# Performance work log

Hardware: AMD Instinct MI355X
Metric: run time of the kernel (lower is better)

Reference implementation:

```python
import jax, jax.numpy as jnp
import numpy as np

NT = 50000  # target nodes
ND = 50000  # drug nodes
E = 800000  # edges per relation
F = 128     # raw feature dim
C = 64      # hidden channels
NEG_SLOPE = 0.2


def _gat(x_src, x_dst, ei, W_src, W_dst, a_src, a_dst, b, n_dst):
    """PyG GATConv (heads=1, add_self_loops=False) forward."""
    hs = x_src @ W_src                      # [Ns, C]
    hd = x_dst @ W_dst                      # [Nd, C]
    alpha_s = hs @ a_src                    # [Ns]
    alpha_d = hd @ a_dst                    # [Nd]
    src, dst = ei[0], ei[1]
    logits = jax.nn.leaky_relu(alpha_s[src] + alpha_d[dst], NEG_SLOPE)  # [E]
    # segment softmax over incoming edges of each dst node
    m = jax.ops.segment_max(logits, dst, num_segments=n_dst)
    ex = jnp.exp(logits - m[dst])
    den = jax.ops.segment_sum(ex, dst, num_segments=n_dst)
    w = ex / (den[dst] + 1e-16)
    out = jax.ops.segment_sum(w[:, None] * hs[src], dst, num_segments=n_dst)
    return out + b


def setup_inputs() -> dict:
    key = jax.random.key(0)
    ks = jax.random.split(key, 32)
    d = {
        "x_target": jax.random.normal(ks[0], (NT, F), jnp.float32),
        "x_drug": jax.random.normal(ks[1], (ND, F), jnp.float32),
        "ei_tt": jax.random.randint(ks[2], (2, E), 0, NT),
        "ei_dt": jnp.stack([jax.random.randint(ks[3], (E,), 0, ND),
                            jax.random.randint(ks[4], (E,), 0, NT)]),
        "ei_dd": jax.random.randint(ks[5], (2, E), 0, ND),
        "ei_td": jnp.stack([jax.random.randint(ks[6], (E,), 0, NT),
                            jax.random.randint(ks[7], (E,), 0, ND)]),
        "W_tt": jax.random.normal(ks[8], (F, C), jnp.float32) * 0.1,
        "att_tt_src": jax.random.normal(ks[9], (C,), jnp.float32) * 0.1,
        "att_tt_dst": jax.random.normal(ks[10], (C,), jnp.float32) * 0.1,
        "b_tt": jnp.zeros((C,), jnp.float32),
        "W_dt_src": jax.random.normal(ks[11], (F, C), jnp.float32) * 0.1,
        "W_dt_dst": jax.random.normal(ks[12], (F, C), jnp.float32) * 0.1,
        "att_dt_src": jax.random.normal(ks[13], (C,), jnp.float32) * 0.1,
        "att_dt_dst": jax.random.normal(ks[14], (C,), jnp.float32) * 0.1,
        "b_dt": jnp.zeros((C,), jnp.float32),
        "W_dd": jax.random.normal(ks[15], (F, C), jnp.float32) * 0.1,
        "att_dd_src": jax.random.normal(ks[16], (C,), jnp.float32) * 0.1,
        "att_dd_dst": jax.random.normal(ks[17], (C,), jnp.float32) * 0.1,
        "b_dd": jnp.zeros((C,), jnp.float32),
        "W_td_src": jax.random.normal(ks[18], (C, C), jnp.float32) * 0.1,
        "W_td_dst": jax.random.normal(ks[19], (F, C), jnp.float32) * 0.1,
        "att_td_src": jax.random.normal(ks[20], (C,), jnp.float32) * 0.1,
        "att_td_dst": jax.random.normal(ks[21], (C,), jnp.float32) * 0.1,
        "b_td": jnp.zeros((C,), jnp.float32),
    }
    return d


def reference(x_target, x_drug, ei_tt, ei_dt, ei_dd, ei_td,
              W_tt, att_tt_src, att_tt_dst, b_tt,
              W_dt_src, W_dt_dst, att_dt_src, att_dt_dst, b_dt,
              W_dd, att_dd_src, att_dd_dst, b_dd,
              W_td_src, W_td_dst, att_td_src, att_td_dst, b_td):
    x_tt = _gat(x_target, x_target, ei_tt, W_tt, W_tt, att_tt_src, att_tt_dst, b_tt, NT)
    x_dt = _gat(x_drug, x_target, ei_dt, W_dt_src, W_dt_dst, att_dt_src, att_dt_dst, b_dt, NT)
    x_target_new = (x_tt + x_dt) * 0.5
    x_dd = _gat(x_drug, x_drug, ei_dd, W_dd, W_dd, att_dd_src, att_dd_dst, b_dd, ND)
    x_td = _gat(x_target_new, x_drug, ei_td, W_td_src, W_td_dst, att_td_src, att_td_dst, b_td, ND)
    x_drug_new = (x_dd + x_td) * 0.5
    return x_target_new, x_drug_new
```

## Files before the change

### kernel.cpp

```cpp
#include <hip/hip_runtime.h>
#include <hip/hip_bf16.h>

typedef __hip_bfloat16 bf16;

typedef __bf16 bf16v8 __attribute__((ext_vector_type(8)));
typedef short  s16v8  __attribute__((ext_vector_type(8)));
typedef float  f32v4  __attribute__((ext_vector_type(4)));

#define NBLK  256
#define NBLKL 8

__device__ __forceinline__ float bf2f(unsigned short u) {
    return __uint_as_float(((unsigned)u) << 16);
}
__device__ __forceinline__ float bflo(unsigned v) {
    return __uint_as_float(v << 16);
}
__device__ __forceinline__ float bfhi(unsigned v) {
    return __uint_as_float(v & 0xFFFF0000u);
}
__device__ __forceinline__ float ldx(const void* p, size_t i, bool f32) {
    return f32 ? ((const float*)p)[i] : bf2f(((const unsigned short*)p)[i]);
}
__device__ __forceinline__ unsigned short f2bfbits(float f) {
    union { bf16 h; unsigned short u; } cv;
    cv.h = __float2bfloat16(f);
    return cv.u;
}
__device__ __forceinline__ float wave_sum(float v) {
    #pragma unroll
    for (int o = 32; o > 0; o >>= 1) v += __shfl_xor(v, o);
    return v;
}
__device__ __forceinline__ int physidx(int l, int NBtot) {
    return (l & (NBLK - 1)) * NBtot + (l >> NBLKL);
}

__global__ void detect_kernel(const unsigned* __restrict__ x, int nwords,
                              int* __restrict__ flag)
{
    __shared__ int cnt;
    if (threadIdx.x == 0) cnt = 0;
    __syncthreads();
    int c = 0;
    for (int i = threadIdx.x; i < nwords; i += blockDim.x) {
        unsigned e = (x[i] >> 23) & 0xFFu;
        if (e >= 100u && e <= 150u) c++;
    }
    atomicAdd(&cnt, c);
    __syncthreads();
    if (threadIdx.x == 0) flag[0] = (2 * cnt > nwords) ? 1 : 0;
}

struct RelSet {
    const int *src0, *dst0, *src1, *dst1, *src2, *dst2, *src3, *dst3;
    int off1, off2, off3, off4;
    int nd0, nd1, nd2, nd3;
};

__device__ __forceinline__ void pick(const RelSet& rs, int e, int& r,
                                     const int*& s, const int*& d, int& le)
{
    if (e < rs.off1)      { r = 0; s = rs.src0; d = rs.dst0; le = e; }
    else if (e < rs.off2) { r = 1; s = rs.src1; d = rs.dst1; le = e - rs.off1; }
    else if (e < rs.off3) { r = 2; s = rs.src2; d = rs.dst2; le = e - rs.off2; }
    else                  { r = 3; s = rs.src3; d = rs.dst3; le = e - rs.off3; }
}
__device__ __forceinline__ int ndst_of(const RelSet& rs, int r)
{
    return r == 0 ? rs.nd0 : r == 1 ? rs.nd1 : r == 2 ? rs.nd2 : rs.nd3;
}

__global__ __launch_bounds__(1024) void pass1_kernel(
    RelSet rs, int* __restrict__ hist, int NBr)
{
    extern __shared__ int lh[];
    const int NBtot = 4 * NBr;
    for (int i = threadIdx.x; i < NBtot; i += 1024) lh[i] = 0;
    __syncthreads();
    for (int e = blockIdx.x * 1024 + threadIdx.x; e < rs.off4; e += NBLK * 1024) {
        int r, le; const int *s, *d;
        pick(rs, e, r, s, d, le);
        atomicAdd(&lh[r * NBr + (d[le] >> 7)], 1);
    }
    __syncthreads();
    for (int i = threadIdx.x; i < NBtot; i += 1024)
        hist[blockIdx.x * NBtot + i] = lh[i];
}

__global__ __launch_bounds__(1024) void gscan_a_kernel(
    int* __restrict__ buf, int n, int NBtot, int* __restrict__ partials)
{
    __shared__ int sh[1024];
    const int t = threadIdx.x;
    const int base = blockIdx.x * 4096 + t * 4;
    int p0 = 0, p1 = 0, p2 = 0, p3 = 0;
    int v0 = 0, v1 = 0, v2 = 0, v3 = 0;
    if (base < n)     { p0 = physidx(base,     NBtot); v0 = buf[p0]; }
    if (base + 1 < n) { p1 = physidx(base + 1, NBtot); v1 = buf[p1]; }
    if (base + 2 < n) { p2 = physidx(base + 2, NBtot); v2 = buf[p2]; }
    if (base + 3 < n) { p3 = physidx(base + 3, NBtot); v3 = buf[p3]; }
    const int tsum = v0 + v1 + v2 + v3;
    sh[t] = tsum;
    __syncthreads();
    for (int o = 1; o < 1024; o <<= 1) {
        int u = (t >= o) ? sh[t - o] : 0;
        __syncthreads();
        sh[t] += u;
        __syncthreads();
    }
    const int texcl = sh[t] - tsum;
    if (base < n)     buf[p0] = texcl;
    if (base + 1 < n) buf[p1] = texcl + v0;
    if (base + 2 < n) buf[p2] = texcl + v0 + v1;
    if (base + 3 < n) buf[p3] = texcl + v0 + v1 + v2;
    if (t == 1023) partials[blockIdx.x] = sh[t];
}

__global__ __launch_bounds__(1024) void gscan_b_kernel(int* __restrict__ partials,
                                                       int nb)
{
    __shared__ int sh[1024];
    const int t = threadIdx.x;
    int v = (t < nb) ? partials[t] : 0;
    sh[t] = v;
    __syncthreads();
    for (int o = 1; o < 1024; o <<= 1) {
        int u = (t >= o) ? sh[t - o] : 0;
        __syncthreads();
        sh[t] += u;
        __syncthreads();
    }
    if (t < nb) partials[t] = sh[t] - v;
}

__global__ void gscan_c_kernel(int* __restrict__ buf,
                               const int* __restrict__ partials, int n, int NBtot)
{
    int l = blockIdx.x * blockDim.x + threadIdx.x;
    if (l < n) buf[physidx(l, NBtot)] += partials[l >> 12];
}

__global__ __launch_bounds__(1024) void scatter_kernel(
    RelSet rs, const int* __restrict__ O, unsigned* __restrict__ temp, int NBr)
{
    extern __shared__ int cur[];
    const int NBtot = 4 * NBr;
    for (int i = threadIdx.x; i < NBtot; i += 1024)
        cur[i] = O[blockIdx.x * NBtot + i];
    __syncthreads();
    for (int e = blockIdx.x * 1024 + threadIdx.x; e < rs.off4; e += NBLK * 1024) {
        int r, le; const int *s, *d;
        pick(rs, e, r, s, d, le);
        int dd = d[le];
        int b = r * NBr + (dd >> 7);
        int pos = atomicAdd(&cur[b], 1);
        temp[pos] = (unsigned)s[le] | ((unsigned)(dd & 127) << 16);
    }
}

__global__ __launch_bounds__(256) void fillb_kernel(
    RelSet rs, const int* __restrict__ O, const unsigned* __restrict__ temp,
    int* __restrict__ rowptr4, unsigned short* __restrict__ esrc4,
    int NBr, int NP, int EP, int TE)
{
    __shared__ int cnt[128];
    __shared__ int cur[128];
    const int b = blockIdx.x;
    const int NBtot = 4 * NBr;
    const int r = b / NBr;
    const int bloc = b - r * NBr;
    const int dbase = bloc << 7;
    const int nd = ndst_of(rs, r);
    const int bstart = O[b];
    const int bend   = (b + 1 < NBtot) ? O[b + 1] : TE;
    const int relstart = O[r * NBr];
    const int relend   = (r + 1 < 4) ? O[(r + 1) * NBr] : TE;
    const int t = threadIdx.x;

    if (t < 128) cnt[t] = 0;
    __syncthreads();
    for (int i = bstart + t; i < bend; i += 256)
        atomicAdd(&cnt[temp[i] >> 16], 1);
    __syncthreads();
    const int orig = (t < 128) ? cnt[t] : 0;
    for (int o = 1; o < 128; o <<= 1) {
        int add = 0;
        if (t < 128 && t >= o) add = cnt[t - o];
        __syncthreads();
        if (t < 128) cnt[t] += add;
        __syncthreads();
    }
    const int bucket_base = bstart - relstart;
    if (t < 128) {
        const int excl = cnt[t] - orig;
        cur[t] = bucket_base + excl;
        const int d = dbase + t;
        if (d < nd) rowptr4[r * (NP + 1) + d] = bucket_base + excl;
    }
    if (t == 0 && bloc == NBr - 1)
        rowptr4[r * (NP + 1) + nd] = relend - relstart;
    __syncthreads();
    unsigned short* es = esrc4 + (size_t)r * EP;
    for (int i = bstart + t; i < bend; i += 256) {
        unsigned u = temp[i];
        int pos = atomicAdd(&cur[u >> 16], 1);
        es[pos] = (unsigned short)(u & 0xFFFFu);
    }
}

__device__ __forceinline__ void pack_one(const void* W, unsigned short* Wp,
                                         int i, bool f32)
{
    int k = i >> 6, c = i & 63;
    int kt = k >> 5, q = (k >> 3) & 3, j = k & 7;
    int ct = c >> 4, n = c & 15;
    Wp[(((kt * 4 + ct) * 64) + q * 16 + n) * 8 + j] = f2bfbits(ldx(W, i, f32));
}

__global__ __launch_bounds__(256) void pack4_kernel(
    const void* __restrict__ W0, const void* __restrict__ W1,
    const void* __restrict__ W2, const void* __restrict__ W3,
    unsigned short* __restrict__ P0, unsigned short* __restrict__ P1,
    unsigned short* __restrict__ P2, unsigned short* __restrict__ P3,
    const int* __restrict__ flag)
{
    const bool f32 = (flag[0] != 0);
    int i = blockIdx.x * 256 + threadIdx.x;
    if (i < 8192)       pack_one(W0, P0, i, f32);
    else if (i < 16384) pack_one(W1, P1, i - 8192, f32);
    else if (i < 24576) pack_one(W2, P2, i - 16384, f32);
    else if (i < 28672) pack_one(W3, P3, i - 24576, f32);
}

__global__ void wvec2_kernel(const void* __restrict__ W1, const void* __restrict__ a1,
                             const void* __restrict__ W2, const void* __restrict__ a2,
                             float* __restrict__ wv1, float* __restrict__ wv2,
                             const int* __restrict__ flag)
{
    const bool f32 = (flag[0] != 0);
    const int t = threadIdx.x;
    const void* W = (t < 128) ? W1 : W2;
    const void* a = (t < 128) ? a1 : a2;
    const int k = t & 127;
    float s = 0.f;
    for (int c = 0; c < 64; ++c) s += ldx(W, (size_t)k * 64 + c, f32) * ldx(a, c, f32);
    ((t < 128) ? wv1 : wv2)[k] = s;
}

struct ProjArg {
    const void* X; const unsigned short* Wp; const void* a1; const void* a2;
    const float* wvx;
    bf16* H; float* al1; float* al2; float* alx;
    int N;
};

template <int K>
__device__ __forceinline__ void proj_body(const ProjArg& P, bool f32,
                                          int bid, int nblocks)
{
    constexpr int NKT = K / 32;
    const int tid = threadIdx.x;
    const int wave = tid >> 6, lane = tid & 63;
    const int quad = lane >> 4, n = lane & 15;

    s16v8 Bf[NKT][4];
    #pragma unroll
    for (int kt = 0; kt < NKT; ++kt)
        #pragma unroll
        for (int ct = 0; ct < 4; ++ct)
            Bf[kt][ct] = *(const s16v8*)&P.Wp[((kt * 4 + ct) * 64 + lane) * 8];

    float a1v[4], a2v[4];
    #pragma unroll
    for (int ct = 0; ct < 4; ++ct) {
        a1v[ct] = P.a1 ? ldx(P.a1, ct * 16 + n, f32) : 0.f;
        a2v[ct] = P.a2 ? ldx(P.a2, ct * 16 + n, f32) : 0.f;
    }
    float wv[NKT][8];
    if (P.wvx) {
        #pragma unroll
        for (int kt = 0; kt < NKT; ++kt)
            #pragma unroll
            for (int j = 0; j < 8; ++j)
                wv[kt][j] = P.wvx[kt * 32 + quad * 8 + j];
    }

    const int tiles = (P.N + 15) / 16;
    for (int tb = bid * 4 + wave; tb < tiles; tb += nblocks * 4) {
        const int r0 = tb * 16;
        const int arow = r0 + n;
        const int ars  = (arow < P.N) ? arow : 0;

        f32v4 acc[4];
        #pragma unroll
        for (int ct = 0; ct < 4; ++ct) acc[ct] = (f32v4){0.f, 0.f, 0.f, 0.f};
        float txd = 0.f;

        #pragma unroll
        for (int kt = 0; kt < NKT; ++kt) {
            s16v8 As;
            if (f32) {
                const float4* xp = (const float4*)P.X +
                    ((size_t)ars * K + kt * 32 + quad * 8) / 4;
                float4 x0 = xp[0], x1 = xp[1];
                As[0] = (short)f2bfbits(x0.x); As[1] = (short)f2bfbits(x0.y);
                As[2] = (short)f2bfbits(x0.z); As[3] = (short)f2bfbits(x0.w);
                As[4] = (short)f2bfbits(x1.x); As[5] = (short)f2bfbits(x1.y);
                As[6] = (short)f2bfbits(x1.z); As[7] = (short)f2bfbits(x1.w);
            } else {
                As = *(const s16v8*)((const unsigned short*)P.X +
                    (size_t)ars * K + kt * 32 + quad * 8);
            }
            if (P.wvx) {
                #pragma unroll
                for (int j = 0; j < 8; ++j)
                    txd = fmaf(bf2f((unsigned short)As[j]), wv[kt][j], txd);
            }
            bf16v8 Ab = __builtin_bit_cast(bf16v8, As);
            #pragma unroll
            for (int ct = 0; ct < 4; ++ct)
                acc[ct] = __builtin_amdgcn_mfma_f32_16x16x32_bf16(
                    Ab, __builtin_bit_cast(bf16v8, Bf[kt][ct]), acc[ct], 0, 0, 0);
        }

        if (P.alx) {
            txd += __shfl_xor(txd, 16);
            txd += __shfl_xor(txd, 32);
            if (lane < 16 && r0 + lane < P.N) P.alx[r0 + lane] = txd;
        }

        #pragma unroll
        for (int i = 0; i < 4; ++i) {
            const int r = r0 + quad * 4 + i;
            const bool rv = (r < P.N);
            if (rv && P.H) {
                #pragma unroll
                for (int ct = 0; ct < 4; ++ct)
                    P.H[(size_t)r * 64 + ct * 16 + n] = __float2bfloat16(acc[ct][i]);
            }
            if (P.al1) {
                float t = acc[0][i] * a1v[0] + acc[1][i] * a1v[1] +
                          acc[2][i] * a1v[2] + acc[3][i] * a1v[3];
                #pragma unroll
                for (int o = 1; o < 16; o <<= 1) t += __shfl_xor(t, o);
                if (rv && n == 0) P.al1[r] = t;
            }
            if (P.al2) {
                float t = acc[0][i] * a2v[0] + acc[1][i] * a2v[1] +
                          acc[2][i] * a2v[2] + acc[3][i] * a2v[3];
                #pragma unroll
                for (int o = 1; o < 16; o <<= 1) t += __shfl_xor(t, o);
                if (rv && n == 0) P.al2[r] = t;
            }
        }
    }
}

template <int KA, int KB, int KC>
__global__ __launch_bounds__(256) void proj3_kernel(ProjArg A, ProjArg B, ProjArg C,
                                                    int nA, int nB,
                                                    const int* __restrict__ flag)
{
    const bool f32 = (flag[0] != 0);
    const int bx = blockIdx.x;
    if (bx < nA)            proj_body<KA>(A, f32, bx, nA);
    else if (bx < nA + nB)  proj_body<KB>(B, f32, bx - nA, nB);
    else                    proj_body<KC>(C, f32, bx - nA - nB,
                                          gridDim.x - nA - nB);
}

template <int K>
__global__ __launch_bounds__(256) void proj1_kernel(ProjArg A,
                                                    const int* __restrict__ flag)
{
    proj_body<K>(A, flag[0] != 0, blockIdx.x, gridDim.x);
}

__global__ __launch_bounds__(256) void agg2_kernel(
    const int* __restrict__ rp1, const unsigned short* __restrict__ es1,
    const unsigned* __restrict__ HS1, const float* __restrict__ als1,
    const float* __restrict__ ald1,
    const int* __restrict__ rp2, const unsigned short* __restrict__ es2,
    const unsigned* __restrict__ HS2, const float* __restrict__ als2,
    const float* __restrict__ ald2,
    const void* __restrict__ b1, const void* __restrict__ b2,
    void* __restrict__ out, size_t out_off, int n, const int* __restrict__ flag)
{
    const int gw   = (blockIdx.x * blockDim.x + threadIdx.x) >> 6;
    const int lane = threadIdx.x & 63;
    if (gw >= n) return;
    const int half = lane >> 5;
    const int ch2  = lane & 31;

    int p1 = rp1[gw], e1 = rp1[gw + 1];
    int p2 = rp2[gw], e2 = rp2[gw + 1];
    const float ad1 = ald1[gw], ad2 = ald2[gw];

    float l1a = 0.f, h1a = 0.f, l1b = 0.f, h1b = 0.f, den1 = 0.f;
    float l2a = 0.f, h2a = 0.f, l2b = 0.f, h2b = 0.f, den2 = 0.f;

    while (p1 < e1 || p2 < e2) {
        int nn1 = e1 - p1; nn1 = nn1 < 0 ? 0 : (nn1 > 64 ? 64 : nn1);
        int nn2 = e2 - p2; nn2 = nn2 < 0 ? 0 : (nn2 > 64 ? 64 : nn2);
        int s1 = 0, s2 = 0; float w1 = 0.f, w2 = 0.f;
        if (lane < nn1) {
            s1 = es1[p1 + lane];
            float l = als1[s1] + ad1;
            l = (l > 0.f) ? l : 0.2f * l;
            w1 = __expf(l);
        }
        if (lane < nn2) {
            s2 = es2[p2 + lane];
            float l = als2[s2] + ad2;
            l = (l > 0.f) ? l : 0.2f * l;
            w2 = __expf(l);
        }
        den1 += w1; den2 += w2;

        const int jm = (nn1 > nn2) ? nn1 : nn2;
        for (int j = 0; j < jm; j += 8) {
            int   sA1 = __shfl(s1, j + half),     sB1 = __shfl(s1, j + 2 + half);
            int   sC1 = __shfl(s1, j + 4 + half), sD1 = __shfl(s1, j + 6 + half);
            float wA1 = __shfl(w1, j + half),     wB1 = __shfl(w1, j + 2 + half);
            float wC1 = __shfl(w1, j + 4 + half), wD1 = __shfl(w1, j + 6 + half);
            int   sA2 = __shfl(s2, j + half),     sB2 = __shfl(s2, j + 2 + half);
            int   sC2 = __shfl(s2, j + 4 + half), sD2 = __shfl(s2, j + 6 + half);
            float wA2 = __shfl(w2, j + half),     wB2 = __shfl(w2, j + 2 + half);
            float wC2 = __shfl(w2, j + 4 + half), wD2 = __shfl(w2, j + 6 + half);
            unsigned vA1 = HS1[(size_t)sA1 * 32 + ch2];
            unsigned vB1 = HS1[(size_t)sB1 * 32 + ch2];
            unsigned vC1 = HS1[(size_t)sC1 * 32 + ch2];
            unsigned vD1 = HS1[(size_t)sD1 * 32 + ch2];
            unsigned vA2 = HS2[(size_t)sA2 * 32 + ch2];
            unsigned vB2 = HS2[(size_t)sB2 * 32 + ch2];
            unsigned vC2 = HS2[(size_t)sC2 * 32 + ch2];
            unsigned vD2 = HS2[(size_t)sD2 * 32 + ch2];
            l1a = fmaf(wA1, bflo(vA1), l1a); h1a = fmaf(wA1, bfhi(vA1), h1a);
            l1b = fmaf(wB1, bflo(vB1), l1b); h1b = fmaf(wB1, bfhi(vB1), h1b);
            l1a = fmaf(wC1, bflo(vC1), l1a); h1a = fmaf(wC1, bfhi(vC1), h1a);
            l1b = fmaf(wD1, bflo(vD1), l1b); h1b = fmaf(wD1, bfhi(vD1), h1b);
            l2a = fmaf(wA2, bflo(vA2), l2a); h2a = fmaf(wA2, bfhi(vA2), h2a);
            l2b = fmaf(wB2, bflo(vB2), l2b); h2b = fmaf(wB2, bfhi(vB2), h2b);
            l2a = fmaf(wC2, bflo(vC2), l2a); h2a = fmaf(wC2, bfhi(vC2), h2a);
            l2b = fmaf(wD2, bflo(vD2), l2b); h2b = fmaf(wD2, bfhi(vD2), h2b);
        }
        p1 += nn1; p2 += nn2;
    }

    float lo1 = l1a + l1b, hi1 = h1a + h1b;
    float lo2 = l2a + l2b, hi2 = h2a + h2b;
    lo1 += __shfl_xor(lo1, 32); hi1 += __shfl_xor(hi1, 32);
    lo2 += __shfl_xor(lo2, 32); hi2 += __shfl_xor(hi2, 32);
    den1 = wave_sum(den1);
    den2 = wave_sum(den2);
    const float inv1 = 1.0f / (den1 + 1e-16f);
    const float inv2 = 1.0f / (den2 + 1e-16f);

    if (half == 0) {
        const bool f32 = (flag[0] != 0);
        const int c0 = 2 * ch2;
        float vlo = 0.5f * (lo1 * inv1 + lo2 * inv2 +
                            ldx(b1, c0, f32) + ldx(b2, c0, f32));
        float vhi = 0.5f * (hi1 * inv1 + hi2 * inv2 +
                            ldx(b1, c0 + 1, f32) + ldx(b2, c0 + 1, f32));
        const size_t pairidx = (out_off >> 1) + (size_t)gw * 32 + ch2;
        if (f32) ((float2*)out)[pairidx] = make_float2(vlo, vhi);
        else {
            ushort2 u2 = make_ushort2(f2bfbits(vlo), f2bfbits(vhi));
            ((ushort2*)out)[pairidx] = u2;
        }
    }
}

extern "C" void kernel_launch(void* const* d_in, const int* in_sizes, int n_in,
                              void* d_out, int out_size, void* d_ws, size_t ws_size,
                              hipStream_t stream)
{
    const void* x_t = d_in[0];
    const void* x_d = d_in[1];
    const int* ei_tt = (const int*)d_in[2];
    const int* ei_dt = (const int*)d_in[3];
    const int* ei_dd = (const int*)d_in[4];
    const int* ei_td = (const int*)d_in[5];
    const void* W_tt     = d_in[6];
    const void* att_tt_s = d_in[7];
    const void* att_tt_d = d_in[8];
    const void* b_tt     = d_in[9];
    const void* W_dt_src = d_in[10];
    const void* W_dt_dst = d_in[11];
    const void* att_dt_s = d_in[12];
    const void* att_dt_d = d_in[13];
    const void* b_dt     = d_in[14];
    const void* W_dd     = d_in[15];
    const void* att_dd_s = d_in[16];
    const void* att_dd_d = d_in[17];
    const void* b_dd     = d_in[18];
    const void* W_td_src = d_in[19];
    const void* W_td_dst = d_in[20];
    const void* att_td_s = d_in[21];
    const void* att_td_d = d_in[22];
    const void* b_td     = d_in[23];

    const int NT = in_sizes[0] / 128;
    const int ND = in_sizes[1] / 128;
    const int Ett = in_sizes[2] / 2, Edt = in_sizes[3] / 2,
              Edd = in_sizes[4] / 2, Etd = in_sizes[5] / 2;
    const int NMAX = (NT > ND) ? NT : ND;
    int EMAX = Ett;
    if (Edt > EMAX) EMAX = Edt;
    if (Edd > EMAX) EMAX = Edd;
    if (Etd > EMAX) EMAX = Etd;
    const int TE = Ett + Edt + Edd + Etd;

    const int NBr  = (NMAX + 127) >> 7;
    const int NBtot = 4 * NBr;
    const int HM = NBtot * NBLK;

    char* wptr = (char*)d_ws;
    auto alloc = [&](size_t bytes) -> void* {
        void* p = (void*)wptr;
        wptr += (bytes + 255) & ~(size_t)255;
        return p;
    };
    bf16*  h1      = (bf16*)alloc((size_t)NMAX * 64 * 2);
    bf16*  h2      = (bf16*)alloc((size_t)NMAX * 64 * 2);
    float* als[4]; float* ald[4];
    for (int r = 0; r < 4; ++r) {
        als[r] = (float*)alloc((size_t)NMAX * 4);
        ald[r] = (float*)alloc((size_t)NMAX * 4);
    }
    int*   hist    = (int*)alloc((size_t)HM * 4);
    int*   rowptr4 = (int*)alloc((size_t)4 * (NMAX + 1) * 4);
    unsigned short* esrc4 = (unsigned short*)alloc((size_t)4 * EMAX * 2);
    unsigned* temp = (unsigned*)alloc((size_t)TE * 4);
    int*   gpart   = (int*)alloc(1024 * 4);
    float* wvec_dt = (float*)alloc(128 * 4);
    float* wvec_td = (float*)alloc(128 * 4);
    unsigned short* wp_tt = (unsigned short*)alloc(8192 * 2);
    unsigned short* wp_dt = (unsigned short*)alloc(8192 * 2);
    unsigned short* wp_dd = (unsigned short*)alloc(8192 * 2);
    unsigned short* wp_td = (unsigned short*)alloc(4096 * 2);
    int*   flag    = (int*)alloc(256 * 4);
    bf16*  h3      = (bf16*)temp;

    RelSet rs;
    rs.src0 = ei_tt; rs.dst0 = ei_tt + Ett;
    rs.src1 = ei_dt; rs.dst1 = ei_dt + Edt;
    rs.src2 = ei_dd; rs.dst2 = ei_dd + Edd;
    rs.src3 = ei_td; rs.dst3 = ei_td + Etd;
    rs.off1 = Ett; rs.off2 = Ett + Edt; rs.off3 = Ett + Edt + Edd; rs.off4 = TE;
    rs.nd0 = NT; rs.nd1 = NT; rs.nd2 = ND; rs.nd3 = ND;

    detect_kernel<<<1, 256, 0, stream>>>((const unsigned*)x_t, 4096, flag);

    pack4_kernel<<<112, 256, 0, stream>>>(W_tt, W_dt_src, W_dd, W_td_src,
                                          wp_tt, wp_dt, wp_dd, wp_td, flag);
    wvec2_kernel<<<1, 256, 0, stream>>>(W_dt_dst, att_dt_d, W_td_dst, att_td_d,
                                        wvec_dt, wvec_td, flag);

    const size_t ldsB = (size_t)NBtot * 4;
    pass1_kernel<<<NBLK, 1024, ldsB, stream>>>(rs, hist, NBr);
    const int gnb = (HM + 4095) / 4096;
    gscan_a_kernel<<<gnb, 1024, 0, stream>>>(hist, HM, NBtot, gpart);
    gscan_b_kernel<<<1, 1024, 0, stream>>>(gpart, gnb);
    gscan_c_kernel<<<(HM + 255) / 256, 256, 0, stream>>>(hist, gpart, HM, NBtot);
    scatter_kernel<<<NBLK, 1024, ldsB, stream>>>(rs, hist, temp, NBr);
    fillb_kernel<<<NBtot, 256, 0, stream>>>(rs, hist, temp, rowptr4, esrc4,
                                            NBr, NMAX, EMAX, TE);

    ProjArg Ptt{ x_t, wp_tt, att_tt_s, att_tt_d, wvec_dt,
                 h1, als[0], ald[0], ald[1], NT };
    ProjArg Pdt{ x_d, wp_dt, att_dt_s, nullptr, wvec_td,
                 h2, als[1], nullptr, ald[3], ND };
    ProjArg Pdd{ x_d, wp_dd, att_dd_s, att_dd_d, nullptr,
                 h3, als[2], ald[2], nullptr, ND };
    proj3_kernel<128, 128, 128><<<2304, 256, 0, stream>>>(Ptt, Pdt, Pdd,
                                                          768, 768, flag);

    agg2_kernel<<<(NT + 3) / 4, 256, 0, stream>>>(
        rowptr4 + 0 * (NMAX + 1), esrc4 + (size_t)0 * EMAX,
        (const unsigned*)h1, als[0], ald[0],
        rowptr4 + 1 * (NMAX + 1), esrc4 + (size_t)1 * EMAX,
        (const unsigned*)h2, als[1], ald[1],
        b_tt, b_dt, d_out, 0, NT, flag);

    ProjArg Ptd{ d_out, wp_td, att_td_s, nullptr, nullptr,
                 h1, als[3], nullptr, nullptr, NT };
    proj1_kernel<64><<<1024, 256, 0, stream>>>(Ptd, flag);

    agg2_kernel<<<(ND + 3) / 4, 256, 0, stream>>>(
        rowptr4 + 2 * (NMAX + 1), esrc4 + (size_t)2 * EMAX,
        (const unsigned*)h3, als[2], ald[2],
        rowptr4 + 3 * (NMAX + 1), esrc4 + (size_t)3 * EMAX,
        (const unsigned*)h1, als[3], ald[3],
        b_dd, b_td, d_out, (size_t)NT * 64, ND, flag);
}
```

Baseline: 337.4 us.

## Replace two-level bucketed CSR build with global atomic counting sort

Result: slower. 625.2 us (+85.3%).

```diff
diff --git a/kernel.cpp b/kernel.cpp
--- a/kernel.cpp
+++ b/kernel.cpp
@@ -6,9 +6,6 @@
 typedef __bf16 bf16v8 __attribute__((ext_vector_type(8)));
 typedef short  s16v8  __attribute__((ext_vector_type(8)));
 typedef float  f32v4  __attribute__((ext_vector_type(4)));
-
-#define NBLK  256
-#define NBLKL 8
 
 __device__ __forceinline__ float bf2f(unsigned short u) {
     return __uint_as_float(((unsigned)u) << 16);
@@ -31,9 +28,6 @@
     #pragma unroll
     for (int o = 32; o > 0; o >>= 1) v += __shfl_xor(v, o);
     return v;
-}
-__device__ __forceinline__ int physidx(int l, int NBtot) {
-    return (l & (NBLK - 1)) * NBtot + (l >> NBLKL);
 }
 
 __global__ void detect_kernel(const unsigned* __restrict__ x, int nwords,
@@ -66,40 +60,34 @@
     else if (e < rs.off3) { r = 2; s = rs.src2; d = rs.dst2; le = e - rs.off2; }
     else                  { r = 3; s = rs.src3; d = rs.dst3; le = e - rs.off3; }
 }
-__device__ __forceinline__ int ndst_of(const RelSet& rs, int r)
-{
-    return r == 0 ? rs.nd0 : r == 1 ? rs.nd1 : r == 2 ? rs.nd2 : rs.nd3;
-}
-
-__global__ __launch_bounds__(1024) void pass1_kernel(
-    RelSet rs, int* __restrict__ hist, int NBr)
-{
-    extern __shared__ int lh[];
-    const int NBtot = 4 * NBr;
-    for (int i = threadIdx.x; i < NBtot; i += 1024) lh[i] = 0;
-    __syncthreads();
-    for (int e = blockIdx.x * 1024 + threadIdx.x; e < rs.off4; e += NBLK * 1024) {
-        int r, le; const int *s, *d;
-        pick(rs, e, r, s, d, le);
-        atomicAdd(&lh[r * NBr + (d[le] >> 7)], 1);
-    }
-    __syncthreads();
-    for (int i = threadIdx.x; i < NBtot; i += 1024)
-        hist[blockIdx.x * NBtot + i] = lh[i];
+
+__global__ void zero_kernel(int* __restrict__ p, int n)
+{
+    int i = blockIdx.x * blockDim.x + threadIdx.x;
+    if (i < n) p[i] = 0;
+}
+
+__global__ __launch_bounds__(1024) void count_kernel(
+    RelSet rs, int* __restrict__ C, int NP1)
+{
+    int e = blockIdx.x * 1024 + threadIdx.x;
+    if (e >= rs.off4) return;
+    int r, le; const int *s, *d;
+    pick(rs, e, r, s, d, le);
+    atomicAdd(&C[r * NP1 + d[le]], 1);
 }
 
 __global__ __launch_bounds__(1024) void gscan_a_kernel(
-    int* __restrict__ buf, int n, int NBtot, int* __restrict__ partials)
+    int* __restrict__ buf, int n, int* __restrict__ partials)
 {
     __shared__ int sh[1024];
     const int t = threadIdx.x;
     const int base = blockIdx.x * 4096 + t * 4;
-    int p0 = 0, p1 = 0, p2 = 0, p3 = 0;
     int v0 = 0, v1 = 0, v2 = 0, v3 = 0;
-    if (base < n)     { p0 = physidx(base,     NBtot); v0 = buf[p0]; }
-    if (base + 1 < n) { p1 = physidx(base + 1, NBtot); v1 = buf[p1]; }
-    if (base + 2 < n) { p2 = physidx(base + 2, NBtot); v2 = buf[p2]; }
-    if (base + 3 < n) { p3 = physidx(base + 3, NBtot); v3 = buf[p3]; }
+    if (base < n)     v0 = buf[base];
+    if (base + 1 < n) v1 = buf[base + 1];
+    if (base + 2 < n) v2 = buf[base + 2];
+    if (base + 3 < n) v3 = buf[base + 3];
     const int tsum = v0 + v1 + v2 + v3;
     sh[t] = tsum;
     __syncthreads();
@@ -110,10 +98,10 @@
         __syncthreads();
     }
     const int texcl = sh[t] - tsum;
-    if (base < n)     buf[p0] = texcl;
-    if (base + 1 < n) buf[p1] = texcl + v0;
-    if (base + 2 < n) buf[p2] = texcl + v0 + v1;
-    if (base + 3 < n) buf[p3] = texcl + v0 + v1 + v2;
+    if (base < n)     buf[base]     = texcl;
+    if (base + 1 < n) buf[base + 1] = texcl + v0;
+    if (base + 2 < n) buf[base + 2] = texcl + v0 + v1;
+    if (base + 3 < n) buf[base + 3] = texcl + v0 + v1 + v2;
     if (t == 1023) partials[blockIdx.x] = sh[t];
 }
 
@@ -134,79 +122,26 @@
     if (t < nb) partials[t] = sh[t] - v;
 }
 
-__global__ void gscan_c_kernel(int* __restrict__ buf,
-                               const int* __restrict__ partials, int n, int NBtot)
+__global__ void gscan_c_kernel(int* __restrict__ buf, int* __restrict__ cur,
+                               const int* __restrict__ partials, int n)
 {
     int l = blockIdx.x * blockDim.x + threadIdx.x;
-    if (l < n) buf[physidx(l, NBtot)] += partials[l >> 12];
-}
-
-__global__ __launch_bounds__(1024) void scatter_kernel(
-    RelSet rs, const int* __restrict__ O, unsigned* __restrict__ temp, int NBr)
-{
-    extern __shared__ int cur[];
-    const int NBtot = 4 * NBr;
-    for (int i = threadIdx.x; i < NBtot; i += 1024)
-        cur[i] = O[blockIdx.x * NBtot + i];
-    __syncthreads();
-    for (int e = blockIdx.x * 1024 + threadIdx.x; e < rs.off4; e += NBLK * 1024) {
-        int r, le; const int *s, *d;
-        pick(rs, e, r, s, d, le);
-        int dd = d[le];
-        int b = r * NBr + (dd >> 7);
-        int pos = atomicAdd(&cur[b], 1);
-        temp[pos] = (unsigned)s[le] | ((unsigned)(dd & 127) << 16);
-    }
-}
-
-__global__ __launch_bounds__(256) void fillb_kernel(
-    RelSet rs, const int* __restrict__ O, const unsigned* __restrict__ temp,
-    int* __restrict__ rowptr4, unsigned short* __restrict__ esrc4,
-    int NBr, int NP, int EP, int TE)
-{
-    __shared__ int cnt[128];
-    __shared__ int cur[128];
-    const int b = blockIdx.x;
-    const int NBtot = 4 * NBr;
-    const int r = b / NBr;
-    const int bloc = b - r * NBr;
-    const int dbase = bloc << 7;
-    const int nd = ndst_of(rs, r);
-    const int bstart = O[b];
-    const int bend   = (b + 1 < NBtot) ? O[b + 1] : TE;
-    const int relstart = O[r * NBr];
-    const int relend   = (r + 1 < 4) ? O[(r + 1) * NBr] : TE;
-    const int t = threadIdx.x;
-
-    if (t < 128) cnt[t] = 0;
-    __syncthreads();
-    for (int i = bstart + t; i < bend; i += 256)
-        atomicAdd(&cnt[temp[i] >> 16], 1);
-    __syncthreads();
-    const int orig = (t < 128) ? cnt[t] : 0;
-    for (int o = 1; o < 128; o <<= 1) {
-        int add = 0;
-        if (t < 128 && t >= o) add = cnt[t - o];
-        __syncthreads();
-        if (t < 128) cnt[t] += add;
-        __syncthreads();
-    }
-    const int bucket_base = bstart - relstart;
-    if (t < 128) {
-        const int excl = cnt[t] - orig;
-        cur[t] = bucket_base + excl;
-        const int d = dbase + t;
-        if (d < nd) rowptr4[r * (NP + 1) + d] = bucket_base + excl;
-    }
-    if (t == 0 && bloc == NBr - 1)
-        rowptr4[r * (NP + 1) + nd] = relend - relstart;
-    __syncthreads();
-    unsigned short* es = esrc4 + (size_t)r * EP;
-    for (int i = bstart + t; i < bend; i += 256) {
-        unsigned u = temp[i];
-        int pos = atomicAdd(&cur[u >> 16], 1);
-        es[pos] = (unsigned short)(u & 0xFFFFu);
-    }
+    if (l < n) {
+        int v = buf[l] + partials[l >> 12];
+        buf[l] = v;
+        cur[l] = v;
+    }
+}
+
+__global__ __launch_bounds__(1024) void place_kernel(
+    RelSet rs, int* __restrict__ cur, unsigned short* __restrict__ es, int NP1)
+{
+    int e = blockIdx.x * 1024 + threadIdx.x;
+    if (e >= rs.off4) return;
+    int r, le; const int *s, *d;
+    pick(rs, e, r, s, d, le);
+    int pos = atomicAdd(&cur[r * NP1 + d[le]], 1);
+    es[pos] = (unsigned short)s[le];
 }
 
 __device__ __forceinline__ void pack_one(const void* W, unsigned short* Wp,
@@ -507,15 +442,9 @@
     const int Ett = in_sizes[2] / 2, Edt = in_sizes[3] / 2,
               Edd = in_sizes[4] / 2, Etd = in_sizes[5] / 2;
     const int NMAX = (NT > ND) ? NT : ND;
-    int EMAX = Ett;
-    if (Edt > EMAX) EMAX = Edt;
-    if (Edd > EMAX) EMAX = Edd;
-    if (Etd > EMAX) EMAX = Etd;
     const int TE = Ett + Edt + Edd + Etd;
-
-    const int NBr  = (NMAX + 127) >> 7;
-    const int NBtot = 4 * NBr;
-    const int HM = NBtot * NBLK;
+    const int NP1 = NMAX + 1;
+    const int CN  = 4 * NP1;
 
     char* wptr = (char*)d_ws;
     auto alloc = [&](size_t bytes) -> void* {
@@ -525,15 +454,15 @@
     };
     bf16*  h1      = (bf16*)alloc((size_t)NMAX * 64 * 2);
     bf16*  h2      = (bf16*)alloc((size_t)NMAX * 64 * 2);
+    bf16*  h3      = (bf16*)alloc((size_t)NMAX * 64 * 2);
     float* als[4]; float* ald[4];
     for (int r = 0; r < 4; ++r) {
         als[r] = (float*)alloc((size_t)NMAX * 4);
         ald[r] = (float*)alloc((size_t)NMAX * 4);
     }
-    int*   hist    = (int*)alloc((size_t)HM * 4);
-    int*   rowptr4 = (int*)alloc((size_t)4 * (NMAX + 1) * 4);
-    unsigned short* esrc4 = (unsigned short*)alloc((size_t)4 * EMAX * 2);
-    unsigned* temp = (unsigned*)alloc((size_t)TE * 4);
+    int*   rowptr4 = (int*)alloc((size_t)CN * 4);
+    int*   cur4    = (int*)alloc((size_t)CN * 4);
+    unsigned short* esrc = (unsigned short*)alloc((size_t)TE * 2);
     int*   gpart   = (int*)alloc(1024 * 4);
     float* wvec_dt = (float*)alloc(128 * 4);
     float* wvec_td = (float*)alloc(128 * 4);
@@ -542,7 +471,6 @@
     unsigned short* wp_dd = (unsigned short*)alloc(8192 * 2);
     unsigned short* wp_td = (unsigned short*)alloc(4096 * 2);
     int*   flag    = (int*)alloc(256 * 4);
-    bf16*  h3      = (bf16*)temp;
 
     RelSet rs;
     rs.src0 = ei_tt; rs.dst0 = ei_tt + Ett;
@@ -559,15 +487,14 @@
     wvec2_kernel<<<1, 256, 0, stream>>>(W_dt_dst, att_dt_d, W_td_dst, att_td_d,
                                         wvec_dt, wvec_td, flag);
 
-    const size_t ldsB = (size_t)NBtot * 4;
-    pass1_kernel<<<NBLK, 1024, ldsB, stream>>>(rs, hist, NBr);
-    const int gnb = (HM + 4095) / 4096;
-    gscan_a_kernel<<<gnb, 1024, 0, stream>>>(hist, HM, NBtot, gpart);
+    zero_kernel<<<(CN + 1023) / 1024, 1024, 0, stream>>>(rowptr4, CN);
+    count_kernel<<<(TE + 1023) / 1024, 1024, 0, stream>>>(rs, rowptr4, NP1);
+    const int gnb = (CN + 4095) / 4096;
+    gscan_a_kernel<<<gnb, 1024, 0, stream>>>(rowptr4, CN, gpart);
     gscan_b_kernel<<<1, 1024, 0, stream>>>(gpart, gnb);
-    gscan_c_kernel<<<(HM + 255) / 256, 256, 0, stream>>>(hist, gpart, HM, NBtot);
-    scatter_kernel<<<NBLK, 1024, ldsB, stream>>>(rs, hist, temp, NBr);
-    fillb_kernel<<<NBtot, 256, 0, stream>>>(rs, hist, temp, rowptr4, esrc4,
-                                            NBr, NMAX, EMAX, TE);
+    gscan_c_kernel<<<(CN + 1023) / 1024, 1024, 0, stream>>>(rowptr4, cur4,
+                                                            gpart, CN);
+    place_kernel<<<(TE + 1023) / 1024, 1024, 0, stream>>>(rs, cur4, esrc, NP1);
 
     ProjArg Ptt{ x_t, wp_tt, att_tt_s, att_tt_d, wvec_dt,
                  h1, als[0], ald[0], ald[1], NT };
@@ -579,9 +506,9 @@
                                                           768, 768, flag);
 
     agg2_kernel<<<(NT + 3) / 4, 256, 0, stream>>>(
-        rowptr4 + 0 * (NMAX + 1), esrc4 + (size_t)0 * EMAX,
+        rowptr4 + 0 * NP1, esrc,
         (const unsigned*)h1, als[0], ald[0],
-        rowptr4 + 1 * (NMAX + 1), esrc4 + (size_t)1 * EMAX,
+        rowptr4 + 1 * NP1, esrc,
         (const unsigned*)h2, als[1], ald[1],
         b_tt, b_dt, d_out, 0, NT, flag);
 
@@ -590,9 +517,9 @@
     proj1_kernel<64><<<1024, 256, 0, stream>>>(Ptd, flag);
 
     agg2_kernel<<<(ND + 3) / 4, 256, 0, stream>>>(
-        rowptr4 + 2 * (NMAX + 1), esrc4 + (size_t)2 * EMAX,
+        rowptr4 + 2 * NP1, esrc,
         (const unsigned*)h3, als[2], ald[2],
-        rowptr4 + 3 * (NMAX + 1), esrc4 + (size_t)3 * EMAX,
+        rowptr4 + 3 * NP1, esrc,
         (const unsigned*)h1, als[3], ald[3],
         b_dd, b_td, d_out, (size_t)NT * 64, ND, flag);
 }
```

## Fuse td source projection into target aggregation epilogue

Applied to the files above, without the earlier changes.

Result: slower. 361.7 us (+7.2%).

```diff
diff --git a/kernel.cpp b/kernel.cpp
--- a/kernel.cpp
+++ b/kernel.cpp
@@ -223,6 +223,7 @@
     const void* __restrict__ W2, const void* __restrict__ W3,
     unsigned short* __restrict__ P0, unsigned short* __restrict__ P1,
     unsigned short* __restrict__ P2, unsigned short* __restrict__ P3,
+    unsigned short* __restrict__ P3p,
     const int* __restrict__ flag)
 {
     const bool f32 = (flag[0] != 0);
@@ -230,7 +231,11 @@
     if (i < 8192)       pack_one(W0, P0, i, f32);
     else if (i < 16384) pack_one(W1, P1, i - 8192, f32);
     else if (i < 24576) pack_one(W2, P2, i - 16384, f32);
-    else if (i < 28672) pack_one(W3, P3, i - 24576, f32);
+    else if (i < 28672) {
+        int ii = i - 24576;
+        pack_one(W3, P3, ii, f32);
+        P3p[ii] = f2bfbits(ldx(W3, ii, f32));
+    }
 }
 
 __global__ void wvec2_kernel(const void* __restrict__ W1, const void* __restrict__ a1,
@@ -370,13 +375,6 @@
                                           gridDim.x - nA - nB);
 }
 
-template <int K>
-__global__ __launch_bounds__(256) void proj1_kernel(ProjArg A,
-                                                    const int* __restrict__ flag)
-{
-    proj_body<K>(A, flag[0] != 0, blockIdx.x, gridDim.x);
-}
-
 __global__ __launch_bounds__(256) void agg2_kernel(
     const int* __restrict__ rp1, const unsigned short* __restrict__ es1,
     const unsigned* __restrict__ HS1, const float* __restrict__ als1,
@@ -385,7 +383,10 @@
     const unsigned* __restrict__ HS2, const float* __restrict__ als2,
     const float* __restrict__ ald2,
     const void* __restrict__ b1, const void* __restrict__ b2,
-    void* __restrict__ out, size_t out_off, int n, const int* __restrict__ flag)
+    void* __restrict__ out, size_t out_off, int n,
+    const unsigned short* __restrict__ Wtd, const void* __restrict__ atd,
+    bf16* __restrict__ Htd, float* __restrict__ alstd,
+    const int* __restrict__ flag)
 {
     const int gw   = (blockIdx.x * blockDim.x + threadIdx.x) >> 6;
     const int lane = threadIdx.x & 63;
@@ -457,19 +458,37 @@
     const float inv1 = 1.0f / (den1 + 1e-16f);
     const float inv2 = 1.0f / (den2 + 1e-16f);
 
+    const bool f32 = (flag[0] != 0);
+    const int c0 = 2 * ch2;
+    const float vlo = 0.5f * (lo1 * inv1 + lo2 * inv2 +
+                              ldx(b1, c0, f32) + ldx(b2, c0, f32));
+    const float vhi = 0.5f * (hi1 * inv1 + hi2 * inv2 +
+                              ldx(b1, c0 + 1, f32) + ldx(b2, c0 + 1, f32));
+
     if (half == 0) {
-        const bool f32 = (flag[0] != 0);
-        const int c0 = 2 * ch2;
-        float vlo = 0.5f * (lo1 * inv1 + lo2 * inv2 +
-                            ldx(b1, c0, f32) + ldx(b2, c0, f32));
-        float vhi = 0.5f * (hi1 * inv1 + hi2 * inv2 +
-                            ldx(b1, c0 + 1, f32) + ldx(b2, c0 + 1, f32));
         const size_t pairidx = (out_off >> 1) + (size_t)gw * 32 + ch2;
         if (f32) ((float2*)out)[pairidx] = make_float2(vlo, vhi);
         else {
             ushort2 u2 = make_ushort2(f2bfbits(vlo), f2bfbits(vhi));
             ((ushort2*)out)[pairidx] = u2;
         }
+    }
+
+    if (Wtd) {
+        const float xl = f32 ? vlo : bf2f(f2bfbits(vlo));
+        const float xh = f32 ? vhi : bf2f(f2bfbits(vhi));
+        float acc = 0.f;
+        #pragma unroll 8
+        for (int j = 0; j < 32; ++j) {
+            float xlj = __shfl(xl, j);
+            float xhj = __shfl(xh, j);
+            acc = fmaf(xlj, bf2f(Wtd[(2 * j) * 64 + lane]), acc);
+            acc = fmaf(xhj, bf2f(Wtd[(2 * j + 1) * 64 + lane]), acc);
+        }
+        Htd[(size_t)gw * 64 + lane] = __float2bfloat16(acc);
+        float t = acc * ldx(atd, lane, f32);
+        t = wave_sum(t);
+        if (lane == 0) alstd[gw] = t;
     }
 }
 
@@ -525,6 +544,7 @@
     };
     bf16*  h1      = (bf16*)alloc((size_t)NMAX * 64 * 2);
     bf16*  h2      = (bf16*)alloc((size_t)NMAX * 64 * 2);
+    bf16*  h4      = (bf16*)alloc((size_t)NMAX * 64 * 2);
     float* als[4]; float* ald[4];
     for (int r = 0; r < 4; ++r) {
         als[r] = (float*)alloc((size_t)NMAX * 4);
@@ -541,6 +561,7 @@
     unsigned short* wp_dt = (unsigned short*)alloc(8192 * 2);
     unsigned short* wp_dd = (unsigned short*)alloc(8192 * 2);
     unsigned short* wp_td = (unsigned short*)alloc(4096 * 2);
+    unsigned short* wp_td_plain = (unsigned short*)alloc(4096 * 2);
     int*   flag    = (int*)alloc(256 * 4);
     bf16*  h3      = (bf16*)temp;
 
@@ -555,7 +576,8 @@
     detect_kernel<<<1, 256, 0, stream>>>((const unsigned*)x_t, 4096, flag);
 
     pack4_kernel<<<112, 256, 0, stream>>>(W_tt, W_dt_src, W_dd, W_td_src,
-                                          wp_tt, wp_dt, wp_dd, wp_td, flag);
+                                          wp_tt, wp_dt, wp_dd, wp_td,
+                                          wp_td_plain, flag);
     wvec2_kernel<<<1, 256, 0, stream>>>(W_dt_dst, att_dt_d, W_td_dst, att_td_d,
                                         wvec_dt, wvec_td, flag);
 
@@ -583,16 +605,14 @@
         (const unsigned*)h1, als[0], ald[0],
         rowptr4 + 1 * (NMAX + 1), esrc4 + (size_t)1 * EMAX,
         (const unsigned*)h2, als[1], ald[1],
-        b_tt, b_dt, d_out, 0, NT, flag);
-
-    ProjArg Ptd{ d_out, wp_td, att_td_s, nullptr, nullptr,
-                 h1, als[3], nullptr, nullptr, NT };
-    proj1_kernel<64><<<1024, 256, 0, stream>>>(Ptd, flag);
+        b_tt, b_dt, d_out, 0, NT,
+        wp_td_plain, att_td_s, h4, als[3], flag);
 
     agg2_kernel<<<(ND + 3) / 4, 256, 0, stream>>>(
         rowptr4 + 2 * (NMAX + 1), esrc4 + (size_t)2 * EMAX,
         (const unsigned*)h3, als[2], ald[2],
         rowptr4 + 3 * (NMAX + 1), esrc4 + (size_t)3 * EMAX,
-        (const unsigned*)h1, als[3], ald[3],
-        b_dd, b_td, d_out, (size_t)NT * 64, ND, flag);
-}
+        (const unsigned*)h4, als[3], ald[3],
+        b_dd, b_td, d_out, (size_t)NT * 64, ND,
+        nullptr, nullptr, nullptr, nullptr, flag);
+}
```
